# Kernel tuning notes

Measured on AMD Instinct MI355X. Metric: run time of the kernel, lower is better.

The kernel has to match this reference:

```python
import jax, jax.numpy as jnp
import numpy as np

HID = 2048
NUM_V, NUM_K = 32, 16
DK, DV = 128, 128
KEY_DIM = NUM_K * DK
VALUE_DIM = NUM_V * DV
CONV_DIM = 2 * KEY_DIM + VALUE_DIM
CONV_K = 4
CHUNK = 64
EPS = 1e-6
B, S = 2, 2048


def setup_inputs():
    key = jax.random.key(0)
    ks = jax.random.split(key, 9)
    w = lambda i, shape, sc=0.02: jax.random.normal(ks[i], shape, jnp.float32) * sc
    return {
        "hidden_states": jax.random.normal(ks[0], (B, S, HID), jnp.float32),
        "W_qkv": w(1, (HID, CONV_DIM)),
        "W_z": w(2, (HID, VALUE_DIM)),
        "W_b": w(3, (HID, NUM_V)),
        "W_a": w(4, (HID, NUM_V)),
        "conv_w": w(5, (CONV_DIM, CONV_K), 0.2),
        "dt_bias": jnp.ones((NUM_V,), jnp.float32),
        "A_log": jnp.log(jax.random.uniform(ks[6], (NUM_V,), jnp.float32, 1e-3, 16.0)),
        "norm_w": jnp.ones((DV,), jnp.float32),
        "W_out": w(7, (VALUE_DIM, HID)),
    }


def _l2norm(x, eps=1e-6):
    return x * jax.lax.rsqrt(jnp.sum(x * x, axis=-1, keepdims=True) + eps)


def _causal_conv_silu(x, w):
    # x: [B, C, S]; depthwise causal conv (kernel K), then SiLU. K is tiny (4).
    K = w.shape[-1]
    xp = jnp.pad(x, ((0, 0), (0, 0), (K - 1, 0)))
    out = sum(xp[:, :, j:j + x.shape[-1]] * w[None, :, j, None] for j in range(K))
    return jax.nn.silu(out)


def _chunk_gated_delta_rule(q, k, v, g, beta, chunk=CHUNK):
    # q,k: [B,S,H,DK]; v: [B,S,H,DV]; g,beta: [B,S,H]. S divisible by chunk.
    q, k = _l2norm(q), _l2norm(k)
    tr = lambda x: jnp.swapaxes(x, 1, 2)
    q, k, v, g, beta = tr(q), tr(k), tr(v), tr(g), tr(beta)  # [B,H,S,...]
    Bb, Hh, Ss, Dk = k.shape
    NC = Ss // chunk
    q = q * (Dk ** -0.5)
    k_beta = k * beta[..., None]
    v_beta = v * beta[..., None]
    ch = lambda x: x.reshape(Bb, Hh, NC, chunk, x.shape[-1])
    q, k, k_beta, v_beta = ch(q), ch(k), ch(k_beta), ch(v_beta)
    g = jnp.cumsum(g.reshape(Bb, Hh, NC, chunk), axis=-1)  # intra-chunk cumulative log-decay
    tril = jnp.tril(jnp.ones((chunk, chunk), bool))
    strict = jnp.tril(jnp.ones((chunk, chunk), bool), -1)
    diff = g[..., :, None] - g[..., None, :]
    dm = jnp.where(tril, jnp.exp(jnp.where(tril, diff, 0.0)), 0.0)  # decay mask, incl. diag
    # strictly-lower A; (I - A) is unit lower triangular -> M = (I - A)^{-1}
    A = -(k_beta @ jnp.swapaxes(k, -1, -2)) * dm * strict
    eye = jnp.eye(chunk, dtype=q.dtype)
    M = jax.scipy.linalg.solve_triangular(eye - A, jnp.broadcast_to(eye, A.shape), lower=True)
    v_c = M @ v_beta
    k_cd = M @ (k_beta * jnp.exp(g)[..., None])

    def step(state, xs):
        q_i, k_i, v_i, g_i, dm_i, kcd_i = xs
        attn_i = (q_i @ jnp.swapaxes(k_i, -1, -2)) * dm_i
        v_new = v_i - kcd_i @ state
        out = (q_i * jnp.exp(g_i)[..., None]) @ state + attn_i @ v_new
        g_last = g_i[..., -1:]
        k_dec = k_i * jnp.exp(g_last - g_i)[..., None]
        state = state * jnp.exp(g_last)[..., None] + jnp.einsum('bhck,bhcv->bhkv', k_dec, v_new)
        return state, out

    mv = lambda x: jnp.moveaxis(x, 2, 0)
    state0 = jnp.zeros((Bb, Hh, Dk, v_c.shape[-1]), q.dtype)
    _, outs = jax.lax.scan(step, state0, (mv(q), mv(k), mv(v_c), mv(g), mv(dm), mv(k_cd)))
    out = jnp.moveaxis(outs, 0, 2).reshape(Bb, Hh, Ss, -1)
    return jnp.swapaxes(out, 1, 2)  # [B,S,H,DV]


def reference(hidden_states, W_qkv, W_z, W_b, W_a, conv_w, dt_bias, A_log, norm_w, W_out):
    Bb, Ss, _ = hidden_states.shape
    mixed = jnp.swapaxes(hidden_states @ W_qkv, 1, 2)  # [B, CONV_DIM, S]
    z = (hidden_states @ W_z).reshape(Bb, Ss, NUM_V, DV)
    beta = jax.nn.sigmoid(hidden_states @ W_b)  # [B,S,NUM_V]
    g = -jnp.exp(A_log) * jax.nn.softplus((hidden_states @ W_a) + dt_bias)
    mixed = _causal_conv_silu(mixed, conv_w)
    mixed = jnp.swapaxes(mixed, 1, 2)  # [B,S,CONV_DIM]
    q = mixed[..., :KEY_DIM].reshape(Bb, Ss, NUM_K, DK)
    k = mixed[..., KEY_DIM:2 * KEY_DIM].reshape(Bb, Ss, NUM_K, DK)
    v = mixed[..., 2 * KEY_DIM:].reshape(Bb, Ss, NUM_V, DV)
    rep = NUM_V // NUM_K
    q = jnp.repeat(q, rep, axis=2)
    k = jnp.repeat(k, rep, axis=2)
    core = _chunk_gated_delta_rule(q, k, v, g, beta)  # [B,S,NUM_V,DV]
    # RMSNormGated: gate with silu(z) before normalization (Mamba2/Qwen3-Next style)
    gated = core * jax.nn.silu(z)
    var = jnp.mean(gated * gated, axis=-1, keepdims=True)
    core = gated * jax.lax.rsqrt(var + EPS) * norm_w
    return core.reshape(Bb, Ss, VALUE_DIM) @ W_out
```

## Files before the change

### kernel.cpp

```cpp
#include <hip/hip_runtime.h>
#include <cstdint>
#include <cstddef>


#define ROWS  4096
#define SEQ   2048
#define HIDN  2048
#define CONVD 8192
#define NWP   12544
#define NUMV  32

using bf16x8 = __attribute__((ext_vector_type(8))) short;
using f32x4v = __attribute__((ext_vector_type(4))) float;

__device__ __forceinline__ float bf2f(unsigned short u) {
  union { unsigned int i; float f; } x; x.i = ((unsigned int)u) << 16; return x.f;
}
__device__ __forceinline__ unsigned short f2bf(float f) {
  union { float f; unsigned int u; } x; x.f = f;
  unsigned int u = x.u;
  unsigned int r = (u + 0x7FFFu + ((u >> 16) & 1u)) >> 16;
  return (unsigned short)r;
}

typedef const __attribute__((address_space(1))) unsigned int GU32;
typedef __attribute__((address_space(3))) unsigned int LU32;
__device__ __forceinline__ void gld_lds16(const void* g, void* l) {
  GU32* gp = (GU32*)(unsigned long long)(uintptr_t)g;
  LU32* lp = (LU32*)(unsigned int)(uintptr_t)l;
  __builtin_amdgcn_global_load_lds(gp, lp, 16, 0, 0);
}
template <int N>
__device__ __forceinline__ void waitcnt_vm() {
  asm volatile("s_waitcnt vmcnt(%0)" ::"i"(N) : "memory");
}

__global__ __launch_bounds__(256) void cast_kernel(const float* __restrict__ in,
                                                   unsigned short* __restrict__ out, int n4) {
  int i = blockIdx.x * 256 + threadIdx.x;
  if (i >= n4) return;
  float4 v = ((const float4*)in)[i];
  ushort4 o;
  o.x = f2bf(v.x); o.y = f2bf(v.y); o.z = f2bf(v.z); o.w = f2bf(v.w);
  ((ushort4*)out)[i] = o;
}

__global__ __launch_bounds__(256) void transpose_kernel(const float* __restrict__ W,
                                                        unsigned short* __restrict__ WT,
                                                        int K, int N, int ld, int roff) {
  __shared__ float tile[64][65];
  const int t = threadIdx.x;
  const int kb = blockIdx.y * 64, nb = blockIdx.x * 64;
  const int r = t >> 2, c0 = (t & 3) * 16;
#pragma unroll
  for (int i = 0; i < 16; ++i) {
    int c = c0 + i;
    float v = 0.f;
    if (nb + c < N) v = W[(size_t)(kb + r) * N + nb + c];
    tile[r][c] = v;
  }
  __syncthreads();
  const int bn = t >> 2;
  if (nb + bn < N) {
#pragma unroll
    for (int i = 0; i < 16; ++i)
      WT[(size_t)(roff + nb + bn) * ld + kb + c0 + i] = f2bf(tile[c0 + i][bn]);
  }
}

template <int BM, int BN, int OUT_BF16>
__global__ __launch_bounds__(512) void gemm_ks_kernel(const unsigned short* __restrict__ Ag,
                                                      const unsigned short* __restrict__ Bg,
                                                      void* __restrict__ Cg, int M, int N, int K) {
  constexpr int PM = BM / 2, PN = BN / 4;
  constexpr int MT = PM / 16, NTF = PN / 16;
  constexpr int NA = BM / 128, NB = BN / 128;
  constexpr int LPS = NA + NB;
  constexpr int REG = (BM + BN) * 64;
  extern __shared__ char lds[];
  const int t = threadIdx.x;
  const int lane = t & 63, wid = t >> 6;
  const int wm = wid >> 2, wn = wid & 3;
  const int rlo = lane & 15, khi = lane >> 4;

  const int gx = gridDim.x, nwg = gx * gridDim.y;
  int id = blockIdx.y * gx + blockIdx.x;
  int sid = (id & 7) * (nwg >> 3) + (id >> 3);
  const int m0 = (sid / gx) * BM, n0 = (sid % gx) * BN;

  const int NT = K >> 6;
  const int NPH = NT * 2;

  const int srow = t >> 2;
  const int scs = ((t & 3) * 16) ^ (((t >> 3) & 3) << 4);
  const char* Ap[NA];
  const char* Bp[NB];
#pragma unroll
  for (int i = 0; i < NA; ++i)
    Ap[i] = (const char*)Ag + (size_t)(m0 + i * 128 + srow) * K * 2 + scs;
#pragma unroll
  for (int i = 0; i < NB; ++i)
    Bp[i] = (const char*)Bg + (size_t)(n0 + i * 128 + srow) * K * 2 + scs;
  char* dst = lds + t * 16;

  int offA[MT], offB[NTF];
#pragma unroll
  for (int mi = 0; mi < MT; ++mi) {
    int o = (wm * PM + mi * 16 + rlo) * 64 + khi * 16;
    o ^= ((o >> 7) & 3) << 4;
    offA[mi] = o;
  }
#pragma unroll
  for (int ni = 0; ni < NTF; ++ni) {
    int o = (wn * PN + ni * 16 + rlo) * 64 + khi * 16;
    o ^= ((o >> 7) & 3) << 4;
    offB[ni] = o + BM * 64;
  }

  f32x4v acc[MT][NTF];
#pragma unroll
  for (int mi = 0; mi < MT; ++mi)
#pragma unroll
    for (int ni = 0; ni < NTF; ++ni) acc[mi][ni] = (f32x4v){0.f, 0.f, 0.f, 0.f};

#define STG(PS)                                                              \
  do {                                                                       \
    int kts_ = ((PS) >> 1 < NT) ? ((PS) >> 1) : NT - 1;                      \
    size_t co_ = (size_t)kts_ * 128 + (size_t)((PS) & 1) * 64;               \
    char* d_ = dst + (((PS) & 3) * REG);                                     \
    _Pragma("unroll") for (int i_ = 0; i_ < NA; ++i_)                        \
        gld_lds16(Ap[i_] + co_, d_ + i_ * 8192);                             \
    _Pragma("unroll") for (int i_ = 0; i_ < NB; ++i_)                        \
        gld_lds16(Bp[i_] + co_, d_ + BM * 64 + i_ * 8192);                   \
  } while (0)

  STG(0); STG(1); STG(2);
  waitcnt_vm<2 * LPS>();
  __builtin_amdgcn_s_barrier();
  __builtin_amdgcn_sched_barrier(0);

#pragma unroll 1
  for (int p = 0; p < NPH; ++p) {
    const char* rb = lds + (p & 3) * REG;
    bf16x8 af[MT], bv[NTF];
#pragma unroll
    for (int mi = 0; mi < MT; ++mi) af[mi] = *(const bf16x8*)(rb + offA[mi]);
#pragma unroll
    for (int ni = 0; ni < NTF; ++ni) bv[ni] = *(const bf16x8*)(rb + offB[ni]);
    STG(p + 3);
    __builtin_amdgcn_s_setprio(1);
#pragma unroll
    for (int mi = 0; mi < MT; ++mi)
#pragma unroll
      for (int ni = 0; ni < NTF; ++ni)
        acc[mi][ni] = __builtin_amdgcn_mfma_f32_16x16x32_bf16(af[mi], bv[ni], acc[mi][ni], 0, 0, 0);
    __builtin_amdgcn_s_setprio(0);
    waitcnt_vm<2 * LPS>();
    __builtin_amdgcn_s_barrier();
    __builtin_amdgcn_sched_barrier(0);
  }
#undef STG
  waitcnt_vm<0>();

  const int mrb = khi * 4;
#pragma unroll
  for (int mi = 0; mi < MT; ++mi)
#pragma unroll
    for (int ni = 0; ni < NTF; ++ni)
#pragma unroll
      for (int r = 0; r < 4; ++r) {
        int mm = m0 + wm * PM + mi * 16 + mrb + r;
        int nn = n0 + wn * PN + ni * 16 + rlo;
        float v = acc[mi][ni][r];
        if (OUT_BF16) ((unsigned short*)Cg)[(size_t)mm * N + nn] = f2bf(v);
        else          ((float*)Cg)[(size_t)mm * N + nn] = v;
      }
}

__global__ __launch_bounds__(256) void conv_silu_kernel(const unsigned short* __restrict__ C1,
                                                        const float* __restrict__ conv_w,
                                                        unsigned short* __restrict__ QKV) {
  int idx = blockIdx.x * 256 + threadIdx.x;
  int row = idx >> 11;
  int c4 = (idx & 2047) << 2;
  int s = row & 2047;
  float4 w0 = *(const float4*)(conv_w + (size_t)(c4 + 0) * 4);
  float4 w1 = *(const float4*)(conv_w + (size_t)(c4 + 1) * 4);
  float4 w2 = *(const float4*)(conv_w + (size_t)(c4 + 2) * 4);
  float4 w3 = *(const float4*)(conv_w + (size_t)(c4 + 3) * 4);
  const float* pw0 = (const float*)&w0;
  const float* pw1 = (const float*)&w1;
  const float* pw2 = (const float*)&w2;
  const float* pw3 = (const float*)&w3;
  float a0 = 0.f, a1 = 0.f, a2 = 0.f, a3 = 0.f;
#pragma unroll
  for (int j = 0; j < 4; ++j) {
    int sr = s - 3 + j;
    if (sr < 0) continue;
    ushort4 mv = *(const ushort4*)(C1 + (size_t)(row - 3 + j) * NWP + c4);
    a0 += bf2f(mv.x) * pw0[j];
    a1 += bf2f(mv.y) * pw1[j];
    a2 += bf2f(mv.z) * pw2[j];
    a3 += bf2f(mv.w) * pw3[j];
  }
  ushort4 o;
  o.x = f2bf(a0 / (1.f + __expf(-a0)));
  o.y = f2bf(a1 / (1.f + __expf(-a1)));
  o.z = f2bf(a2 / (1.f + __expf(-a2)));
  o.w = f2bf(a3 / (1.f + __expf(-a3)));
  *(ushort4*)(QKV + (size_t)row * CONVD + c4) = o;
}

__global__ __launch_bounds__(256) void gbeta_kernel(const unsigned short* __restrict__ C1,
                                                    const float* __restrict__ dt_bias,
                                                    const float* __restrict__ A_log,
                                                    float* __restrict__ G, float* __restrict__ BETA) {
  int idx = blockIdx.x * 256 + threadIdx.x;
  int row = idx >> 5, h = idx & 31;
  float bp = bf2f(C1[(size_t)row * NWP + 12288 + h]);
  float ap = bf2f(C1[(size_t)row * NWP + 12320 + h]);
  BETA[idx] = 1.f / (1.f + __expf(-bp));
  float x = ap + dt_bias[h];
  float sp = (x > 15.f) ? x : log1pf(__expf(x));
  G[idx] = -__expf(A_log[h]) * sp;
}

#define INTRA_SMEM 70144
__global__ __launch_bounds__(256) void intra_kernel(const unsigned short* __restrict__ QKV,
                                                    const float* __restrict__ G,
                                                    const float* __restrict__ BETA,
                                                    unsigned short* __restrict__ WU,
                                                    unsigned short* __restrict__ ATTN) {
  extern __shared__ char smem[];
  unsigned short* ktb = (unsigned short*)smem;
  float* Amat = (float*)(smem + 17408);
  float* Xt   = (float*)(smem + 34816);
  unsigned short* qb = (unsigned short*)Xt;
  float* gc  = (float*)(smem + 69632);
  float* bet = gc + 64;

  const int t = threadIdx.x;
  const int lane = t & 63, w = t >> 6;
  const int rlo = lane & 15, khi = lane >> 4;
  const int cix = blockIdx.x & 31;
  const int h = (blockIdx.x >> 5) & 31;
  const int b = blockIdx.x >> 10;
  const int hq = h >> 1;
  const int row0 = cix * 64;
  const size_t rowbase = (size_t)b * SEQ;

  if (t < 64) {
    float gv = G[(rowbase + row0 + t) * NUMV + h];
    bet[t] = BETA[(rowbase + row0 + t) * NUMV + h];
#pragma unroll
    for (int off = 1; off < 64; off <<= 1) {
      float u = __shfl_up(gv, off, 64);
      if (t >= off) gv += u;
    }
    gc[t] = gv;
  }
  __syncthreads();

  const int r = t >> 2, q4 = t & 3;
  const size_t grow = (rowbase + row0 + r) * (size_t)CONVD;

  {
    const unsigned short* kp = QKV + grow + 2048 + hq * 128 + q4 * 32;
    float kv[32]; float ssk = 0.f;
#pragma unroll
    for (int j = 0; j < 32; j += 4) {
      ushort4 km = *(const ushort4*)(kp + j);
      kv[j] = bf2f(km.x); kv[j + 1] = bf2f(km.y); kv[j + 2] = bf2f(km.z); kv[j + 3] = bf2f(km.w);
      ssk += kv[j]*kv[j] + kv[j+1]*kv[j+1] + kv[j+2]*kv[j+2] + kv[j+3]*kv[j+3];
    }
    ssk += __shfl_xor(ssk, 1, 64);
    ssk += __shfl_xor(ssk, 2, 64);
    const float rk = rsqrtf(ssk + 1e-6f);
    const float ekr = __expf(gc[r]) * bet[r];
#pragma unroll
    for (int j = 0; j < 32; ++j) {
      float kn = kv[j] * rk;
      ktb[r * 136 + q4 * 32 + j] = f2bf(kn);
      Xt[(q4 * 32 + j) * 68 + r] = kn * ekr;
    }
  }
  __syncthreads();

  float xr[64];

  {
    static const signed char SJ[10][2] = {{0,0},{1,0},{1,1},{2,0},{2,1},{2,2},{3,0},{3,1},{3,2},{3,3}};
    static const signed char SB[5] = {0, 4, 7, 9, 10};
    for (int sj = SB[w]; sj < SB[w + 1]; ++sj) {
      const int mt = SJ[sj][0], nt = SJ[sj][1];
      f32x4v acc = (f32x4v){0.f, 0.f, 0.f, 0.f};
#pragma unroll
      for (int ks = 0; ks < 4; ++ks) {
        bf16x8 af = *(const bf16x8*)&ktb[(mt * 16 + rlo) * 136 + ks * 32 + khi * 8];
        bf16x8 bf_ = *(const bf16x8*)&ktb[(nt * 16 + rlo) * 136 + ks * 32 + khi * 8];
        acc = __builtin_amdgcn_mfma_f32_16x16x32_bf16(af, bf_, acc, 0, 0, 0);
      }
      const int j = nt * 16 + rlo;
#pragma unroll
      for (int r2 = 0; r2 < 4; ++r2) {
        const int i = mt * 16 + khi * 4 + r2;
        if (j < i) Amat[i * 68 + j] = -bet[i] * __expf(gc[i] - gc[j]) * acc[r2];
      }
    }
    if (t < 128) {
      const float* Xc = Xt + t * 68;
#pragma unroll
      for (int j = 0; j < 64; j += 4) {
        f32x4v xv = *(const f32x4v*)(Xc + j);
        xr[j] = xv[0]; xr[j + 1] = xv[1]; xr[j + 2] = xv[2]; xr[j + 3] = xv[3];
      }
    }
  }
  __syncthreads();

  {
    const unsigned short* vp = QKV + grow + 4096 + h * 128 + q4 * 32;
    const float brow = bet[r];
#pragma unroll
    for (int j = 0; j < 32; j += 4) {
      ushort4 vm = *(const ushort4*)(vp + j);
      Xt[(q4 * 32 + j + 0) * 68 + r] = bf2f(vm.x) * brow;
      Xt[(q4 * 32 + j + 1) * 68 + r] = bf2f(vm.y) * brow;
      Xt[(q4 * 32 + j + 2) * 68 + r] = bf2f(vm.z) * brow;
      Xt[(q4 * 32 + j + 3) * 68 + r] = bf2f(vm.w) * brow;
    }
  }
  __syncthreads();
  if (t >= 128) {
    const float* Xc = Xt + (t - 128) * 68;
#pragma unroll
    for (int j = 0; j < 64; j += 4) {
      f32x4v xv = *(const f32x4v*)(Xc + j);
      xr[j] = xv[0]; xr[j + 1] = xv[1]; xr[j + 2] = xv[2]; xr[j + 3] = xv[3];
    }
  }
  __syncthreads();

#pragma unroll
  for (int ib = 0; ib < 8; ++ib) {
    const int i0 = ib * 8;
    float p[8] = {0, 0, 0, 0, 0, 0, 0, 0};
#pragma unroll
    for (int j = 0; j < i0; j += 4) {
#pragma unroll
      for (int r2 = 0; r2 < 8; ++r2) {
        f32x4v ar = *(const f32x4v*)&Amat[(i0 + r2) * 68 + j];
        p[r2] += ar[0] * xr[j] + ar[1] * xr[j + 1] + ar[2] * xr[j + 2] + ar[3] * xr[j + 3];
      }
    }
#pragma unroll
    for (int r2 = 0; r2 < 8; ++r2) {
      float v = xr[i0 + r2] + p[r2];
#pragma unroll
      for (int r3 = 0; r3 < r2; ++r3) v += Amat[(i0 + r2) * 68 + i0 + r3] * xr[i0 + r3];
      xr[i0 + r2] = v;
    }
  }

  if (t < 128) {
    float* Xc = Xt + t * 68;
#pragma unroll
    for (int j = 0; j < 64; j += 4) {
      f32x4v xv = {xr[j], xr[j + 1], xr[j + 2], xr[j + 3]};
      *(f32x4v*)(Xc + j) = xv;
    }
  }
  __syncthreads();
  {
    unsigned short* wdst = WU + (rowbase + row0 + r) * (size_t)NWP + h * 128 + q4 * 32;
#pragma unroll
    for (int j = 0; j < 32; ++j) wdst[j] = f2bf(Xt[(q4 * 32 + j) * 68 + r]);
  }
  __syncthreads();
  if (t >= 128) {
    float* Xc = Xt + (t - 128) * 68;
#pragma unroll
    for (int j = 0; j < 64; j += 4) {
      f32x4v xv = {xr[j], xr[j + 1], xr[j + 2], xr[j + 3]};
      *(f32x4v*)(Xc + j) = xv;
    }
  }
  __syncthreads();
  {
    unsigned short* udst = WU + (rowbase + row0 + r) * (size_t)NWP + 4096 + h * 128 + q4 * 32;
#pragma unroll
    for (int j = 0; j < 32; ++j) udst[j] = f2bf(Xt[(q4 * 32 + j) * 68 + r]);
  }
  __syncthreads();

  {
    const unsigned short* qp = QKV + grow + hq * 128 + q4 * 32;
    float qv[32]; float ssq = 0.f;
#pragma unroll
    for (int j = 0; j < 32; j += 4) {
      ushort4 qm = *(const ushort4*)(qp + j);
      qv[j] = bf2f(qm.x); qv[j + 1] = bf2f(qm.y); qv[j + 2] = bf2f(qm.z); qv[j + 3] = bf2f(qm.w);
      ssq += qv[j]*qv[j] + qv[j+1]*qv[j+1] + qv[j+2]*qv[j+2] + qv[j+3]*qv[j+3];
    }
    ssq += __shfl_xor(ssq, 1, 64);
    ssq += __shfl_xor(ssq, 2, 64);
    const float rq = rsqrtf(ssq + 1e-6f) * 0.08838834764831845f;
#pragma unroll
    for (int j = 0; j < 32; ++j) qb[r * 136 + q4 * 32 + j] = f2bf(qv[j] * rq);
  }
  __syncthreads();

  {
    const size_t abase = (((size_t)b * 32 + h) * 32 + cix) * 4096;
#pragma unroll 1
    for (int nt = 0; nt < 4; ++nt) {
      const int j = nt * 16 + rlo;
      float vals[4] = {0.f, 0.f, 0.f, 0.f};
      if (nt <= w) {
        f32x4v acc = (f32x4v){0.f, 0.f, 0.f, 0.f};
#pragma unroll
        for (int ks = 0; ks < 4; ++ks) {
          bf16x8 af = *(const bf16x8*)&qb[(w * 16 + rlo) * 136 + ks * 32 + khi * 8];
          bf16x8 bf_ = *(const bf16x8*)&ktb[(nt * 16 + rlo) * 136 + ks * 32 + khi * 8];
          acc = __builtin_amdgcn_mfma_f32_16x16x32_bf16(af, bf_, acc, 0, 0, 0);
        }
#pragma unroll
        for (int r2 = 0; r2 < 4; ++r2) {
          const int i = w * 16 + khi * 4 + r2;
          if (j <= i) vals[r2] = __expf(gc[i] - gc[j]) * acc[r2];
        }
      }
#pragma unroll
      for (int r2 = 0; r2 < 4; ++r2)
        ATTN[abase + (w * 16 + khi * 4 + r2) * 64 + j] = f2bf(vals[r2]);
    }
  }
}

#define SEQ_SMEM 70400
__global__ __launch_bounds__(256) void seq_kernel(const unsigned short* __restrict__ QKV,
                                                  const float* __restrict__ G,
                                                  const unsigned short* __restrict__ WU,
                                                  const unsigned short* __restrict__ ATTN,
                                                  unsigned short* __restrict__ CORE) {
  extern __shared__ char smem[];
  unsigned short* ktT    = (unsigned short*)smem;
  unsigned short* wb     = (unsigned short*)(smem + 22528);
  unsigned short* attnb  = (unsigned short*)(smem + 39936);
  float* stateT          = (float*)(smem + 51200);
  unsigned short* stateTb = (unsigned short*)(smem + 59904);
  unsigned short* vnTb   = (unsigned short*)(smem + 64256);
  unsigned short* vdTb   = (unsigned short*)(smem + 67072);
  float* gc   = (float*)(smem + 69888);
  float* edec = (float*)(smem + 70144);

  const int t = threadIdx.x;
  const int lane = t & 63, w = t >> 6;
  const int rlo = lane & 15, khi = lane >> 4;
  const int vq = blockIdx.x & 7;
  const int h = (blockIdx.x >> 3) & 31;
  const int b = blockIdx.x >> 8;
  const int hq = h >> 1;
  const size_t rowbase = (size_t)b * SEQ;
  const size_t ahead = ((size_t)b * 32 + h) * 32;

  for (int i = t; i < 16 * 136; i += 256) { stateT[i] = 0.f; stateTb[i] = 0; }
  __syncthreads();

  bf16x8 qf[4];

#pragma unroll 1
  for (int ncb = 0; ncb < 32; ++ncb) {
    const int row0 = ncb * 64;

    if (t < 64) {
      float gv = G[(rowbase + row0 + t) * NUMV + h];
#pragma unroll
      for (int off = 1; off < 64; off <<= 1) {
        float u = __shfl_up(gv, off, 64);
        if (t >= off) gv += u;
      }
      gc[t] = gv;
      float tot = __shfl(gv, 63, 64);
      edec[t] = __expf(tot - gv);
    }
    __syncthreads();

    {
      const int r = t >> 2, q4 = t & 3;
      const size_t grow = (rowbase + row0 + r) * (size_t)CONVD;
      const unsigned short* kp = QKV + grow + 2048 + hq * 128 + q4 * 32;
      float kv[32]; float ssk = 0.f;
#pragma unroll
      for (int j = 0; j < 32; j += 4) {
        ushort4 km = *(const ushort4*)(kp + j);
        kv[j] = bf2f(km.x); kv[j + 1] = bf2f(km.y); kv[j + 2] = bf2f(km.z); kv[j + 3] = bf2f(km.w);
        ssk += kv[j]*kv[j] + kv[j+1]*kv[j+1] + kv[j+2]*kv[j+2] + kv[j+3]*kv[j+3];
      }
      ssk += __shfl_xor(ssk, 1, 64);
      ssk += __shfl_xor(ssk, 2, 64);
      const float rk = rsqrtf(ssk + 1e-6f);
#pragma unroll
      for (int j = 0; j < 32; ++j) ktT[(q4 * 32 + j) * 88 + r] = f2bf(kv[j] * rk);
      const unsigned short* wsrc = WU + (rowbase + row0 + r) * (size_t)NWP + h * 128 + q4 * 32;
#pragma unroll
      for (int u2 = 0; u2 < 4; ++u2)
        *(uint4*)&wb[r * 136 + q4 * 32 + u2 * 8] = *(const uint4*)(wsrc + u2 * 8);
      const unsigned short* asrc = ATTN + (ahead + ncb) * 4096 + r * 64 + q4 * 16;
      *(uint4*)&attnb[r * 88 + q4 * 16] = *(const uint4*)(asrc);
      *(uint4*)&attnb[r * 88 + q4 * 16 + 8] = *(const uint4*)(asrc + 8);
      const unsigned short* qsrc = QKV + (rowbase + row0 + w * 16 + rlo) * (size_t)CONVD + hq * 128 + khi * 8;
      float qv[32]; float ssq = 0.f;
#pragma unroll
      for (int ks = 0; ks < 4; ++ks) {
        ushort4 qa = *(const ushort4*)(qsrc + ks * 32);
        ushort4 qb2 = *(const ushort4*)(qsrc + ks * 32 + 4);
        qv[ks*8+0] = bf2f(qa.x); qv[ks*8+1] = bf2f(qa.y); qv[ks*8+2] = bf2f(qa.z); qv[ks*8+3] = bf2f(qa.w);
        qv[ks*8+4] = bf2f(qb2.x); qv[ks*8+5] = bf2f(qb2.y); qv[ks*8+6] = bf2f(qb2.z); qv[ks*8+7] = bf2f(qb2.w);
#pragma unroll
        for (int e = 0; e < 8; ++e) ssq += qv[ks*8+e] * qv[ks*8+e];
      }
      ssq += __shfl_xor(ssq, 16, 64);
      ssq += __shfl_xor(ssq, 32, 64);
      const float rq = rsqrtf(ssq + 1e-6f) * 0.08838834764831845f;
#pragma unroll
      for (int ks = 0; ks < 4; ++ks) {
        bf16x8 tv;
#pragma unroll
        for (int e = 0; e < 8; ++e) tv[e] = (short)f2bf(qv[ks*8+e] * rq);
        qf[ks] = tv;
      }
    }
    __syncthreads();

    f32x4v oacc;
    {
      f32x4v pacc = (f32x4v){0.f, 0.f, 0.f, 0.f};
      oacc = (f32x4v){0.f, 0.f, 0.f, 0.f};
#pragma unroll
      for (int ks = 0; ks < 4; ++ks) {
        bf16x8 aw = *(const bf16x8*)&wb[(w * 16 + rlo) * 136 + ks * 32 + khi * 8];
        bf16x8 bs = *(const bf16x8*)&stateTb[rlo * 136 + ks * 32 + khi * 8];
        pacc = __builtin_amdgcn_mfma_f32_16x16x32_bf16(aw, bs, pacc, 0, 0, 0);
        oacc = __builtin_amdgcn_mfma_f32_16x16x32_bf16(qf[ks], bs, oacc, 0, 0, 0);
      }
#pragma unroll
      for (int r2 = 0; r2 < 4; ++r2) {
        const int i = w * 16 + khi * 4 + r2;
        float uv = bf2f(WU[(rowbase + row0 + i) * (size_t)NWP + 4096 + h * 128 + vq * 16 + rlo]);
        float vn = uv - pacc[r2];
        vnTb[rlo * 88 + i] = f2bf(vn);
        vdTb[rlo * 88 + i] = f2bf(vn * edec[i]);
        oacc[r2] *= __expf(gc[i]);
      }
    }
    __syncthreads();

    {
#pragma unroll
      for (int ks = 0; ks < 2; ++ks) {
        bf16x8 aa = *(const bf16x8*)&attnb[(w * 16 + rlo) * 88 + ks * 32 + khi * 8];
        bf16x8 bv = *(const bf16x8*)&vnTb[rlo * 88 + ks * 32 + khi * 8];
        oacc = __builtin_amdgcn_mfma_f32_16x16x32_bf16(aa, bv, oacc, 0, 0, 0);
      }
      const int col = h * 128 + vq * 16 + rlo;
#pragma unroll
      for (int r2 = 0; r2 < 4; ++r2) {
        const int i = w * 16 + khi * 4 + r2;
        CORE[(rowbase + row0 + i) * (size_t)4096 + col] = f2bf(oacc[r2]);
      }
      const float egl = __expf(gc[63]);
#pragma unroll
      for (int n2 = 0; n2 < 2; ++n2) {
        const int dt = w * 2 + n2;
        f32x4v sacc = (f32x4v){0.f, 0.f, 0.f, 0.f};
#pragma unroll
        for (int ks = 0; ks < 2; ++ks) {
          bf16x8 ak = *(const bf16x8*)&ktT[(dt * 16 + rlo) * 88 + ks * 32 + khi * 8];
          bf16x8 bv2 = *(const bf16x8*)&vdTb[rlo * 88 + ks * 32 + khi * 8];
          sacc = __builtin_amdgcn_mfma_f32_16x16x32_bf16(ak, bv2, sacc, 0, 0, 0);
        }
#pragma unroll
        for (int r2 = 0; r2 < 4; ++r2) {
          const int d = dt * 16 + khi * 4 + r2;
          float ns = stateT[rlo * 136 + d] * egl + sacc[r2];
          stateT[rlo * 136 + d] = ns;
          stateTb[rlo * 136 + d] = f2bf(ns);
        }
      }
    }
    __syncthreads();
  }
}

__global__ __launch_bounds__(256) void gatenorm_kernel(const unsigned short* __restrict__ CORE,
                                                       const unsigned short* __restrict__ C1,
                                                       const float* __restrict__ norm_w,
                                                       unsigned short* __restrict__ NRM) {
  const int wid = blockIdx.x * 4 + (threadIdx.x >> 6);
  const int lane = threadIdx.x & 63;
  const int row = wid >> 5, h = wid & 31;
  const int c = lane * 2;
  const size_t cidx = (size_t)row * 4096 + h * 128 + c;
  const size_t zidx = (size_t)row * NWP + 8192 + h * 128 + c;
  float g0 = bf2f(CORE[cidx]), g1 = bf2f(CORE[cidx + 1]);
  float z0 = bf2f(C1[zidx]), z1 = bf2f(C1[zidx + 1]);
  g0 *= z0 / (1.f + __expf(-z0));
  g1 *= z1 / (1.f + __expf(-z1));
  float ss = g0 * g0 + g1 * g1;
#pragma unroll
  for (int m = 1; m < 64; m <<= 1) ss += __shfl_xor(ss, m, 64);
  const float rr = rsqrtf(ss * (1.f / 128.f) + 1e-6f);
  unsigned int o = ((unsigned int)f2bf(g1 * rr * norm_w[c + 1]) << 16) | (unsigned int)f2bf(g0 * rr * norm_w[c]);
  *(unsigned int*)(NRM + cidx) = o;
}

extern "C" void kernel_launch(void* const* d_in, const int* in_sizes, int n_in,
                              void* d_out, int out_size, void* d_ws, size_t ws_size,
                              hipStream_t stream) {
  const float* hs      = (const float*)d_in[0];
  const float* W_qkv   = (const float*)d_in[1];
  const float* W_z     = (const float*)d_in[2];
  const float* W_b     = (const float*)d_in[3];
  const float* W_a     = (const float*)d_in[4];
  const float* conv_w  = (const float*)d_in[5];
  const float* dt_bias = (const float*)d_in[6];
  const float* A_log   = (const float*)d_in[7];
  const float* norm_w  = (const float*)d_in[8];
  const float* W_out   = (const float*)d_in[9];
  float* out = (float*)d_out;
  char* ws = (char*)d_ws;

  const size_t OFF_HSB = 0;
  const size_t OFF_WT  = OFF_HSB + (size_t)ROWS * HIDN * 2;
  const size_t OFF_WOT = OFF_WT + (size_t)NWP * HIDN * 2;
  const size_t OFF_C1  = OFF_WOT + (size_t)HIDN * 4096 * 2;
  const size_t OFF_QKV = OFF_C1 + (size_t)ROWS * NWP * 2;
  const size_t OFF_G   = OFF_QKV + (size_t)ROWS * CONVD * 2;
  const size_t OFF_B   = OFF_G + (size_t)ROWS * NUMV * 4;

  unsigned short* hsb = (unsigned short*)(ws + OFF_HSB);
  unsigned short* WT  = (unsigned short*)(ws + OFF_WT);
  unsigned short* WoT = (unsigned short*)(ws + OFF_WOT);
  unsigned short* C1  = (unsigned short*)(ws + OFF_C1);
  unsigned short* QKV = (unsigned short*)(ws + OFF_QKV);
  float* Gb = (float*)(ws + OFF_G);
  float* Bb = (float*)(ws + OFF_B);
  unsigned short* ATTNb = (unsigned short*)(ws + OFF_HSB);
  unsigned short* COREb = (unsigned short*)(ws + OFF_WT);
  unsigned short* NRMb  = (unsigned short*)(ws + OFF_QKV);

  cast_kernel<<<ROWS * HIDN / 4 / 256, 256, 0, stream>>>(hs, hsb, ROWS * HIDN / 4);
  transpose_kernel<<<dim3(8192 / 64, 2048 / 64), 256, 0, stream>>>(W_qkv, WT, 2048, 8192, HIDN, 0);
  transpose_kernel<<<dim3(4096 / 64, 2048 / 64), 256, 0, stream>>>(W_z, WT, 2048, 4096, HIDN, 8192);
  transpose_kernel<<<dim3(1, 2048 / 64), 256, 0, stream>>>(W_b, WT, 2048, 32, HIDN, 12288);
  transpose_kernel<<<dim3(1, 2048 / 64), 256, 0, stream>>>(W_a, WT, 2048, 32, HIDN, 12320);
  hipMemsetAsync(ws + OFF_WT + (size_t)12352 * HIDN * 2, 0, (size_t)192 * HIDN * 2, stream);
  transpose_kernel<<<dim3(2048 / 64, 4096 / 64), 256, 0, stream>>>(W_out, WoT, 4096, 2048, 4096, 0);

  void (*g1p)(const unsigned short*, const unsigned short*, void*, int, int, int) = gemm_ks_kernel<256, 256, 1>;
  void (*g0p)(const unsigned short*, const unsigned short*, void*, int, int, int) = gemm_ks_kernel<128, 256, 0>;
  hipFuncSetAttribute((const void*)g1p, hipFuncAttributeMaxDynamicSharedMemorySize, 4 * (256 + 256) * 64);
  hipFuncSetAttribute((const void*)g0p, hipFuncAttributeMaxDynamicSharedMemorySize, 4 * (128 + 256) * 64);

  gemm_ks_kernel<256, 256, 1><<<dim3(NWP / 256, ROWS / 256), 512, 4 * (256 + 256) * 64, stream>>>(
      hsb, WT, C1, ROWS, NWP, HIDN);
  conv_silu_kernel<<<ROWS * (CONVD / 4) / 256, 256, 0, stream>>>(C1, conv_w, QKV);
  gbeta_kernel<<<ROWS * NUMV / 256, 256, 0, stream>>>(C1, dt_bias, A_log, Gb, Bb);

  hipFuncSetAttribute((const void*)intra_kernel, hipFuncAttributeMaxDynamicSharedMemorySize,
                      INTRA_SMEM);
  intra_kernel<<<2048, 256, INTRA_SMEM, stream>>>(QKV, Gb, Bb, C1, ATTNb);

  hipFuncSetAttribute((const void*)seq_kernel, hipFuncAttributeMaxDynamicSharedMemorySize,
                      SEQ_SMEM);
  seq_kernel<<<512, 256, SEQ_SMEM, stream>>>(QKV, Gb, C1, ATTNb, COREb);

  gatenorm_kernel<<<ROWS * NUMV / 4, 256, 0, stream>>>(COREb, C1, norm_w, NRMb);
  gemm_ks_kernel<128, 256, 0><<<dim3(2048 / 256, ROWS / 128), 512, 4 * (128 + 256) * 64, stream>>>(
      NRMb, WoT, out, ROWS, 2048, 4096);
}
```

Baseline: 815.3 us.

## Use 5-stage LDS ring pipeline for input GEMM, batch conv rows, vectorize transpose

The big input projection GEMM gets a new kernel variant with a five-slot LDS ring buffer. It prefetches three half-tiles ahead and processes two phases per barrier, aiming to hide global-to-LDS latency and halve the barrier count. The causal conv kernel now makes each thread produce 8 consecutive rows from 11 loaded rows, so it no longer re-reads overlapping inputs. The transpose store uses 16-byte vector writes. The costs are more LDS per block (160KB) and more registers in the conv kernel.

```diff
diff --git a/kernel.cpp b/kernel.cpp
--- a/kernel.cpp
+++ b/kernel.cpp
@@ -60,12 +60,149 @@
     tile[r][c] = v;
   }
   __syncthreads();
-  const int bn = t >> 2;
+  const int bn = t >> 2, seg = (t & 3) * 16;
   if (nb + bn < N) {
-#pragma unroll
-    for (int i = 0; i < 16; ++i)
-      WT[(size_t)(roff + nb + bn) * ld + kb + c0 + i] = f2bf(tile[c0 + i][bn]);
-  }
+    unsigned short tmp[16];
+#pragma unroll
+    for (int i = 0; i < 16; ++i) tmp[i] = f2bf(tile[seg + i][bn]);
+    unsigned short* dst = WT + (size_t)(roff + nb + bn) * ld + kb + seg;
+    *(uint4*)dst = *(const uint4*)&tmp[0];
+    *(uint4*)(dst + 8) = *(const uint4*)&tmp[8];
+  }
+}
+
+template <int BM, int BN, int OUT_BF16>
+__global__ __launch_bounds__(512) void gemm_r5_kernel(const unsigned short* __restrict__ Ag,
+                                                      const unsigned short* __restrict__ Bg,
+                                                      void* __restrict__ Cg, int M, int N, int K) {
+  constexpr int PM = BM / 2, PN = BN / 4;
+  constexpr int MT = PM / 16, NTF = PN / 16;
+  constexpr int NA = BM / 128, NB = BN / 128;
+  constexpr int LPS = NA + NB;
+  constexpr int REG = (BM + BN) * 64;
+  extern __shared__ char lds[];
+  const int t = threadIdx.x;
+  const int lane = t & 63, wid = t >> 6;
+  const int wm = wid >> 2, wn = wid & 3;
+  const int rlo = lane & 15, khi = lane >> 4;
+
+  const int gx = gridDim.x, nwg = gx * gridDim.y;
+  int id = blockIdx.y * gx + blockIdx.x;
+  int sid = (id & 7) * (nwg >> 3) + (id >> 3);
+  const int m0 = (sid / gx) * BM, n0 = (sid % gx) * BN;
+
+  const int NT = K >> 6;
+  const int NPH = NT * 2;
+
+  const int srow = t >> 2;
+  const int scs = ((t & 3) * 16) ^ (((t >> 3) & 3) << 4);
+  const char* Ap[NA];
+  const char* Bp[NB];
+#pragma unroll
+  for (int i = 0; i < NA; ++i)
+    Ap[i] = (const char*)Ag + (size_t)(m0 + i * 128 + srow) * K * 2 + scs;
+#pragma unroll
+  for (int i = 0; i < NB; ++i)
+    Bp[i] = (const char*)Bg + (size_t)(n0 + i * 128 + srow) * K * 2 + scs;
+  char* dst = lds + t * 16;
+
+  int offA[MT], offB[NTF];
+#pragma unroll
+  for (int mi = 0; mi < MT; ++mi) {
+    int o = (wm * PM + mi * 16 + rlo) * 64 + khi * 16;
+    o ^= ((o >> 7) & 3) << 4;
+    offA[mi] = o;
+  }
+#pragma unroll
+  for (int ni = 0; ni < NTF; ++ni) {
+    int o = (wn * PN + ni * 16 + rlo) * 64 + khi * 16;
+    o ^= ((o >> 7) & 3) << 4;
+    offB[ni] = o + BM * 64;
+  }
+
+  f32x4v acc[MT][NTF];
+#pragma unroll
+  for (int mi = 0; mi < MT; ++mi)
+#pragma unroll
+    for (int ni = 0; ni < NTF; ++ni) acc[mi][ni] = (f32x4v){0.f, 0.f, 0.f, 0.f};
+
+#define STG(PS, R)                                                           \
+  do {                                                                       \
+    int kts_ = ((PS) >> 1 < NT) ? ((PS) >> 1) : NT - 1;                      \
+    size_t co_ = (size_t)kts_ * 128 + (size_t)((PS) & 1) * 64;               \
+    char* d_ = dst + (size_t)(R) * REG;                                      \
+    _Pragma("unroll") for (int i_ = 0; i_ < NA; ++i_)                        \
+        gld_lds16(Ap[i_] + co_, d_ + i_ * 8192);                             \
+    _Pragma("unroll") for (int i_ = 0; i_ < NB; ++i_)                        \
+        gld_lds16(Bp[i_] + co_, d_ + BM * 64 + i_ * 8192);                   \
+  } while (0)
+
+  STG(0, 0); STG(1, 1); STG(2, 2);
+  waitcnt_vm<LPS>();
+  __builtin_amdgcn_s_barrier();
+  __builtin_amdgcn_sched_barrier(0);
+
+  int rA = 0;
+#pragma unroll 1
+  for (int q = 0; q < NPH / 2; ++q) {
+    const int p0 = q * 2;
+    int rB = rA + 1; if (rB >= 5) rB -= 5;
+    int tA = rA + 3; if (tA >= 5) tA -= 5;
+    int tB = rA + 4; if (tB >= 5) tB -= 5;
+
+    {
+      const char* rb = lds + (size_t)rA * REG;
+      bf16x8 af[MT], bv[NTF];
+#pragma unroll
+      for (int mi = 0; mi < MT; ++mi) af[mi] = *(const bf16x8*)(rb + offA[mi]);
+#pragma unroll
+      for (int ni = 0; ni < NTF; ++ni) bv[ni] = *(const bf16x8*)(rb + offB[ni]);
+      STG(p0 + 3, tA);
+      __builtin_amdgcn_s_setprio(1);
+#pragma unroll
+      for (int mi = 0; mi < MT; ++mi)
+#pragma unroll
+        for (int ni = 0; ni < NTF; ++ni)
+          acc[mi][ni] = __builtin_amdgcn_mfma_f32_16x16x32_bf16(af[mi], bv[ni], acc[mi][ni], 0, 0, 0);
+      __builtin_amdgcn_s_setprio(0);
+    }
+    {
+      const char* rb = lds + (size_t)rB * REG;
+      bf16x8 af[MT], bv[NTF];
+#pragma unroll
+      for (int mi = 0; mi < MT; ++mi) af[mi] = *(const bf16x8*)(rb + offA[mi]);
+#pragma unroll
+      for (int ni = 0; ni < NTF; ++ni) bv[ni] = *(const bf16x8*)(rb + offB[ni]);
+      STG(p0 + 4, tB);
+      __builtin_amdgcn_s_setprio(1);
+#pragma unroll
+      for (int mi = 0; mi < MT; ++mi)
+#pragma unroll
+        for (int ni = 0; ni < NTF; ++ni)
+          acc[mi][ni] = __builtin_amdgcn_mfma_f32_16x16x32_bf16(af[mi], bv[ni], acc[mi][ni], 0, 0, 0);
+      __builtin_amdgcn_s_setprio(0);
+    }
+    waitcnt_vm<LPS>();
+    __builtin_amdgcn_s_barrier();
+    __builtin_amdgcn_sched_barrier(0);
+    rA += 2; if (rA >= 5) rA -= 5;
+  }
+#undef STG
+  waitcnt_vm<0>();
+
+  const int mrb = khi * 4;
+#pragma unroll
+  for (int mi = 0; mi < MT; ++mi)
+#pragma unroll
+    for (int ni = 0; ni < NTF; ++ni)
+#pragma unroll
+      for (int r = 0; r < 4; ++r) {
+        int mm = m0 + wm * PM + mi * 16 + mrb + r;
+        int nn = n0 + wn * PN + ni * 16 + rlo;
+        float v = acc[mi][ni][r];
+        if (OUT_BF16) ((unsigned short*)Cg)[(size_t)mm * N + nn] = f2bf(v);
+        else          ((float*)Cg)[(size_t)mm * N + nn] = v;
+      }
 }
 
 template <int BM, int BN, int OUT_BF16>
@@ -181,9 +318,10 @@
                                                         const float* __restrict__ conv_w,
                                                         unsigned short* __restrict__ QKV) {
   int idx = blockIdx.x * 256 + threadIdx.x;
-  int row = idx >> 11;
+  int nb = idx >> 11;
   int c4 = (idx & 2047) << 2;
-  int s = row & 2047;
+  int row0 = nb * 8;
+  int s0 = row0 & 2047;
   float4 w0 = *(const float4*)(conv_w + (size_t)(c4 + 0) * 4);
   float4 w1 = *(const float4*)(conv_w + (size_t)(c4 + 1) * 4);
   float4 w2 = *(const float4*)(conv_w + (size_t)(c4 + 2) * 4);
@@ -192,23 +330,30 @@
   const float* pw1 = (const float*)&w1;
   const float* pw2 = (const float*)&w2;
   const float* pw3 = (const float*)&w3;
-  float a0 = 0.f, a1 = 0.f, a2 = 0.f, a3 = 0.f;
-#pragma unroll
-  for (int j = 0; j < 4; ++j) {
-    int sr = s - 3 + j;
-    if (sr < 0) continue;
-    ushort4 mv = *(const ushort4*)(C1 + (size_t)(row - 3 + j) * NWP + c4);
-    a0 += bf2f(mv.x) * pw0[j];
-    a1 += bf2f(mv.y) * pw1[j];
-    a2 += bf2f(mv.z) * pw2[j];
-    a3 += bf2f(mv.w) * pw3[j];
-  }
-  ushort4 o;
-  o.x = f2bf(a0 / (1.f + __expf(-a0)));
-  o.y = f2bf(a1 / (1.f + __expf(-a1)));
-  o.z = f2bf(a2 / (1.f + __expf(-a2)));
-  o.w = f2bf(a3 / (1.f + __expf(-a3)));
-  *(ushort4*)(QKV + (size_t)row * CONVD + c4) = o;
+  ushort4 rw[11];
+#pragma unroll
+  for (int i = 0; i < 11; ++i) {
+    if (s0 + i >= 3) rw[i] = *(const ushort4*)(C1 + (size_t)(row0 - 3 + i) * NWP + c4);
+    else { rw[i].x = 0; rw[i].y = 0; rw[i].z = 0; rw[i].w = 0; }
+  }
+#pragma unroll
+  for (int j = 0; j < 8; ++j) {
+    float a0 = 0.f, a1 = 0.f, a2 = 0.f, a3 = 0.f;
+#pragma unroll
+    for (int jj = 0; jj < 4; ++jj) {
+      ushort4 mv = rw[j + jj];
+      a0 += bf2f(mv.x) * pw0[jj];
+      a1 += bf2f(mv.y) * pw1[jj];
+      a2 += bf2f(mv.z) * pw2[jj];
+      a3 += bf2f(mv.w) * pw3[jj];
+    }
+    ushort4 o;
+    o.x = f2bf(a0 / (1.f + __expf(-a0)));
+    o.y = f2bf(a1 / (1.f + __expf(-a1)));
+    o.z = f2bf(a2 / (1.f + __expf(-a2)));
+    o.w = f2bf(a3 / (1.f + __expf(-a3)));
+    *(ushort4*)(QKV + (size_t)(row0 + j) * CONVD + c4) = o;
+  }
 }
 
 __global__ __launch_bounds__(256) void gbeta_kernel(const unsigned short* __restrict__ C1,
@@ -658,14 +803,14 @@
   hipMemsetAsync(ws + OFF_WT + (size_t)12352 * HIDN * 2, 0, (size_t)192 * HIDN * 2, stream);
   transpose_kernel<<<dim3(2048 / 64, 4096 / 64), 256, 0, stream>>>(W_out, WoT, 4096, 2048, 4096, 0);
 
-  void (*g1p)(const unsigned short*, const unsigned short*, void*, int, int, int) = gemm_ks_kernel<256, 256, 1>;
+  void (*g1p)(const unsigned short*, const unsigned short*, void*, int, int, int) = gemm_r5_kernel<256, 256, 1>;
   void (*g0p)(const unsigned short*, const unsigned short*, void*, int, int, int) = gemm_ks_kernel<128, 256, 0>;
-  hipFuncSetAttribute((const void*)g1p, hipFuncAttributeMaxDynamicSharedMemorySize, 4 * (256 + 256) * 64);
+  hipFuncSetAttribute((const void*)g1p, hipFuncAttributeMaxDynamicSharedMemorySize, 5 * (256 + 256) * 64);
   hipFuncSetAttribute((const void*)g0p, hipFuncAttributeMaxDynamicSharedMemorySize, 4 * (128 + 256) * 64);
 
-  gemm_ks_kernel<256, 256, 1><<<dim3(NWP / 256, ROWS / 256), 512, 4 * (256 + 256) * 64, stream>>>(
+  gemm_r5_kernel<256, 256, 1><<<dim3(NWP / 256, ROWS / 256), 512, 5 * (256 + 256) * 64, stream>>>(
       hsb, WT, C1, ROWS, NWP, HIDN);
-  conv_silu_kernel<<<ROWS * (CONVD / 4) / 256, 256, 0, stream>>>(C1, conv_w, QKV);
+  conv_silu_kernel<<<(ROWS / 8) * 2048 / 256, 256, 0, stream>>>(C1, conv_w, QKV);
   gbeta_kernel<<<ROWS * NUMV / 256, 256, 0, stream>>>(C1, dt_bias, A_log, Gb, Bb);
 
   hipFuncSetAttribute((const void*)intra_kernel, hipFuncAttributeMaxDynamicSharedMemorySize,
```

After: 740.0 us. -9.2%, faster.
